# Kernel tuning notes

Measured on AMD Instinct MI355X. Metric: run time of the kernel, lower is better.

## Reference

```python
import jax, jax.numpy as jnp
import numpy as np

B, N, H, D = 8, 1024, 16, 64
HD = H * D

def setup_inputs() -> dict:
    key = jax.random.key(0)
    ks = jax.random.split(key, 7)
    return {
        "hidden_states": jax.random.normal(ks[0], (B, N, HD), dtype=jnp.float32),
        "qkv_w": jax.random.normal(ks[1], (3 * HD, HD), dtype=jnp.float32) * (HD ** -0.5),
        "q_bias": jax.random.normal(ks[2], (1, 1, HD), dtype=jnp.float32) * 0.02,
        "v_bias": jax.random.normal(ks[3], (1, 1, HD), dtype=jnp.float32) * 0.02,
        "rel_pos": jax.random.normal(ks[4], (1, H, N, N), dtype=jnp.float32),
        "rel_2d_pos": jax.random.normal(ks[5], (1, H, N, N), dtype=jnp.float32),
        "attention_mask": jax.random.randint(ks[6], (B, 1, 1, N), 0, 2, dtype=jnp.int32),
    }

def reference(hidden_states, qkv_w, q_bias, v_bias, rel_pos, rel_2d_pos, attention_mask):
    # fast_qkv path: fused projection, no bias in linear, then add q/v biases
    qkv = jnp.einsum("bnh,oh->bno", hidden_states, qkv_w)  # [B,N,3*HD]
    q, k, v = jnp.split(qkv, 3, axis=-1)
    q = q + q_bias
    v = v + v_bias

    def to_heads(x):  # [B,N,HD] -> [B,H,N,D]
        return x.reshape(B, N, H, D).transpose(0, 2, 1, 3)

    qh = to_heads(q) / jnp.sqrt(jnp.float32(D))
    kh = to_heads(k)
    vh = to_heads(v)

    scores = jnp.einsum("bhnd,bhmd->bhnm", qh, kh)  # [B,H,N,N]
    scores = scores + rel_pos + rel_2d_pos
    # torch mask_fill_ with value 1e-8 (NOT -inf) where mask is True
    scores = jnp.where(attention_mask.astype(bool), jnp.float32(1e-8), scores)
    probs = jax.nn.softmax(scores.astype(jnp.float32), axis=-1).astype(vh.dtype)
    # dropout prob = 0.0 (eval): identity
    ctx = jnp.einsum("bhnm,bhmd->bhnd", probs, vh)  # [B,H,N,D]
    ctx = ctx.transpose(0, 2, 1, 3).reshape(B, N, HD)
    return ctx
```

## Files before the change

### kernel.cpp

```cpp
#include <hip/hip_runtime.h>


typedef __bf16 bf16;
typedef __bf16 bf16x8 __attribute__((ext_vector_type(8)));
typedef __bf16 bf16x4 __attribute__((ext_vector_type(4)));
typedef float floatx4 __attribute__((ext_vector_type(4)));

#define MFMA16(a, b, c) __builtin_amdgcn_mfma_f32_16x16x32_bf16((a), (b), (c), 0, 0, 0)

#define LOG2E 1.4426950408889634f

#define GK(key) ((((key) ^ ((key) >> 3)) & 3) | (((((key) >> 2) ^ ((key) >> 3)) & 1) << 2))

__device__ __forceinline__ void gld16(const bf16* g, bf16* l) {
    __builtin_amdgcn_global_load_lds(
        (const __attribute__((address_space(1))) unsigned int*)g,
        (__attribute__((address_space(3))) unsigned int*)l, 16, 0, 0);
}

__global__ __launch_bounds__(256) void cvt_kernel(const float* __restrict__ x,
                                                  bf16* __restrict__ y, int n4) {
    int i = blockIdx.x * blockDim.x + threadIdx.x;
    if (i >= n4) return;
    float4 v = ((const float4*)x)[i];
    bf16x4 o;
    o.x = (bf16)v.x; o.y = (bf16)v.y; o.z = (bf16)v.z; o.w = (bf16)v.w;
    ((bf16x4*)y)[i] = o;
}

__global__ __launch_bounds__(256) void combine_kernel(const float* __restrict__ a,
                                                      const float* __restrict__ b,
                                                      bf16* __restrict__ y, int n4) {
    int i = blockIdx.x * blockDim.x + threadIdx.x;
    if (i >= n4) return;
    float4 va = ((const float4*)a)[i];
    float4 vb = ((const float4*)b)[i];
    bf16x4 o;
    o.x = (bf16)((va.x + vb.x) * LOG2E); o.y = (bf16)((va.y + vb.y) * LOG2E);
    o.z = (bf16)((va.z + vb.z) * LOG2E); o.w = (bf16)((va.w + vb.w) * LOG2E);
    ((bf16x4*)y)[i] = o;
}

__global__ __launch_bounds__(256) void mask64_kernel(const int* __restrict__ m,
                                                     unsigned long long* __restrict__ om64) {
    int tid = blockIdx.x * blockDim.x + threadIdx.x;
    int gw = tid >> 6, lane = tid & 63;
    bool keep = (m[gw * 64 + lane] == 0);
    unsigned long long bal = __ballot(keep);
    if (lane == 0) om64[gw] = bal;
}

__global__ __launch_bounds__(256) void qkv_gemm(
    const bf16* __restrict__ X, const bf16* __restrict__ W,
    const float* __restrict__ qbias, const float* __restrict__ vbias,
    bf16* __restrict__ qbuf, bf16* __restrict__ kbuf, bf16* __restrict__ vbuf) {
    __shared__ __align__(16) bf16 Al[128 * 32];
    __shared__ __align__(16) bf16 Bl[128 * 32];

    int tid = threadIdx.x, lane = tid & 63, w = tid >> 6;
    int quad = lane >> 4, lcol = lane & 15;
    int bx = blockIdx.x;
    int by = blockIdx.y;
    int wr = w >> 1, wc = w & 1;

    floatx4 z4 = {0.f, 0.f, 0.f, 0.f};
    floatx4 acc[4][4];
    for (int i = 0; i < 4; ++i)
        for (int j = 0; j < 4; ++j) acc[i][j] = z4;

    const bf16* Ag = X + (size_t)by * 128 * 1024;
    const bf16* Bg = W + (size_t)bx * 128 * 1024;

    for (int kt = 0; kt < 32; ++kt) {
        int k0 = kt * 32;
        __syncthreads();
        for (int j = 0; j < 2; ++j) {
            int c = (w * 2 + j) * 64 + lane;
            int row = c >> 2;
            int dc = (c & 3) ^ (row & 3);
            gld16(Ag + (size_t)row * 1024 + k0 + dc * 8, &Al[(w * 2 + j) * 64 * 8]);
        }
        for (int j = 0; j < 2; ++j) {
            int c = (w * 2 + j) * 64 + lane;
            int row = c >> 2;
            int dc = (c & 3) ^ (row & 3);
            gld16(Bg + (size_t)row * 1024 + k0 + dc * 8, &Bl[(w * 2 + j) * 64 * 8]);
        }
        __syncthreads();

        bf16x8 af[4], bfr[4];
        for (int i = 0; i < 4; ++i) {
            int r = wr * 64 + i * 16 + lcol;
            af[i] = *(const bf16x8*)&Al[r * 32 + ((quad ^ (r & 3)) * 8)];
        }
        for (int j = 0; j < 4; ++j) {
            int r = wc * 64 + j * 16 + lcol;
            bfr[j] = *(const bf16x8*)&Bl[r * 32 + ((quad ^ (r & 3)) * 8)];
        }
        for (int i = 0; i < 4; ++i)
            for (int j = 0; j < 4; ++j) acc[i][j] = MFMA16(af[i], bfr[j], acc[i][j]);
    }

    int col0 = bx * 128 + wc * 64;
    int row0 = by * 128 + wr * 64;
    int seg = col0 >> 10;

    for (int i = 0; i < 4; ++i) {
        int m0 = row0 + i * 16 + quad * 4;
        int bb = m0 >> 10, n0 = m0 & 1023;
        for (int j = 0; j < 4; ++j) {
            int o = col0 + j * 16 + lcol;
            if (seg == 0) {
                int hh = o >> 6, d = o & 63;
                float qb = qbias[o];
                for (int r = 0; r < 4; ++r) {
                    float v = (acc[i][j][r] + qb) * (0.125f * LOG2E);
                    qbuf[((size_t)((bb * 16 + hh) * 1024 + n0 + r)) * 64 + d] = (bf16)v;
                }
            } else if (seg == 1) {
                int o2 = o - 1024;
                int hh = o2 >> 6, d = o2 & 63;
                for (int r = 0; r < 4; ++r) {
                    kbuf[((size_t)((bb * 16 + hh) * 1024 + n0 + r)) * 64 + d] = (bf16)acc[i][j][r];
                }
            } else {
                int o2 = o - 2048;
                int hh = o2 >> 6, d = o2 & 63;
                float vbv = vbias[o2];
                bf16x4 pk;
                pk.x = (bf16)(acc[i][j][0] + vbv);
                pk.y = (bf16)(acc[i][j][1] + vbv);
                pk.z = (bf16)(acc[i][j][2] + vbv);
                pk.w = (bf16)(acc[i][j][3] + vbv);
                *(bf16x4*)&vbuf[((size_t)((bb * 16 + hh) * 64 + d)) * 1024 + n0] = pk;
            }
        }
    }
}

__global__ __launch_bounds__(256, 4) void flash_attn(
    const bf16* __restrict__ qbuf, const bf16* __restrict__ kbuf,
    const bf16* __restrict__ vbuf, const bf16* __restrict__ bias,
    const unsigned long long* __restrict__ om64, float* __restrict__ out) {
    __shared__ __align__(16) bf16 Kl[2][64 * 64];
    __shared__ __align__(16) bf16 Vl[2][64 * 64];

    int tid = threadIdx.x, lane = tid & 63, w = tid >> 6;
    int quad = lane >> 4, lcol = lane & 15;
    int bx = blockIdx.x;
    int xcd = bx & 7, slot = bx >> 3;
    int pair = xcd * 32 + (slot >> 3);
    int b = slot & 7;
    int h = pair >> 4, q4 = pair & 15;

    const bf16* kb = kbuf + ((size_t)((b * 16 + h) * 1024)) * 64;
    const bf16* vb = vbuf + ((size_t)((b * 16 + h) * 64)) * 1024;
    const unsigned long long* mp = om64 + b * 16;

    int qrow = q4 * 64 + w * 16;
    const bf16* qp = qbuf + ((size_t)((b * 16 + h) * 1024 + qrow + lcol)) * 64;
    bf16x8 qf0 = *(const bf16x8*)(qp + quad * 8);
    bf16x8 qf1 = *(const bf16x8*)(qp + 32 + quad * 8);
    const bf16* bb = bias + (size_t)h * 1024 * 1024 + (size_t)(qrow + lcol) * 1024;

    floatx4 z4 = {0.f, 0.f, 0.f, 0.f};
    floatx4 oacc[4] = {z4, z4, z4, z4};
    float lrun = 0.f;

#pragma unroll
    for (int j = 0; j < 2; ++j) {
        int c = (w * 2 + j) * 64 + lane;
        int key = c >> 3;
        int dc = (c & 7) ^ GK(key);
        gld16(kb + (size_t)key * 64 + dc * 8, &Kl[0][(w * 2 + j) * 512]);
    }
#pragma unroll
    for (int j = 0; j < 2; ++j) {
        int c = (w * 2 + j) * 64 + lane;
        int d = c >> 3;
        int kc = (c & 7) ^ (d & 7);
        gld16(vb + (size_t)d * 1024 + kc * 8, &Vl[0][(w * 2 + j) * 512]);
    }

    bf16x4 bf_[4];
#pragma unroll
    for (int j = 0; j < 4; ++j) {
        int kboff = ((j >> 1) << 5) + (quad << 3) + ((j & 1) << 2);
        bf_[j] = *(const bf16x4*)(bb + kboff);
    }
    unsigned long long mcur = mp[0];

    for (int kt = 0; kt < 16; ++kt) {
        int k0 = kt * 64;
        int cur = kt & 1, nxt = cur ^ 1;
        __syncthreads();

        if (kt < 15) {
            int k1 = k0 + 64;
#pragma unroll
            for (int j = 0; j < 2; ++j) {
                int c = (w * 2 + j) * 64 + lane;
                int key = c >> 3;
                int dc = (c & 7) ^ GK(key);
                gld16(kb + (size_t)(k1 + key) * 64 + dc * 8, &Kl[nxt][(w * 2 + j) * 512]);
            }
#pragma unroll
            for (int j = 0; j < 2; ++j) {
                int c = (w * 2 + j) * 64 + lane;
                int d = c >> 3;
                int kc = (c & 7) ^ (d & 7);
                gld16(vb + (size_t)d * 1024 + k1 + kc * 8, &Vl[nxt][(w * 2 + j) * 512]);
            }
        }
        int kp = (kt < 15) ? k0 + 64 : 0;
        bf16x4 bn[4];
#pragma unroll
        for (int j = 0; j < 4; ++j) {
            int kboff = ((j >> 1) << 5) + (quad << 3) + ((j & 1) << 2);
            bn[j] = *(const bf16x4*)(bb + kp + kboff);
        }
        unsigned long long mn = mp[(kt < 15) ? kt + 1 : 0];

        floatx4 sacc[4];
#pragma unroll
        for (int j = 0; j < 4; ++j) {
            int key = ((j >> 1) << 5) + ((lcol >> 2) << 3) + ((j & 1) << 2) + (lcol & 3);
            int gk = GK(key);
            bf16x8 kf0 = *(const bf16x8*)&Kl[cur][key * 64 + ((quad ^ gk) * 8)];
            bf16x8 kf1 = *(const bf16x8*)&Kl[cur][key * 64 + (((4 + quad) ^ gk) * 8)];
            floatx4 binit;
            binit[0] = (float)bf_[j][0]; binit[1] = (float)bf_[j][1];
            binit[2] = (float)bf_[j][2]; binit[3] = (float)bf_[j][3];
            sacc[j] = MFMA16(kf0, qf0, binit);
            sacc[j] = MFMA16(kf1, qf1, sacc[j]);
        }

        unsigned int mbits = ((unsigned int)(mcur >> (8 * quad)) & 0xffu) |
                             (((unsigned int)(mcur >> (32 + 8 * quad)) & 0xffu) << 8);
        float p[4][4];
        float psum = 0.f;
#pragma unroll
        for (int j = 0; j < 4; ++j)
#pragma unroll
            for (int r = 0; r < 4; ++r) {
                float sv = ((mbits >> (j * 4 + r)) & 1u) ? sacc[j][r] : 0.f;
                p[j][r] = __builtin_amdgcn_exp2f(sv);
                psum += p[j][r];
            }
        lrun += psum;

        bf16x8 pf0, pf1;
        pf0[0] = (bf16)p[0][0]; pf0[1] = (bf16)p[0][1];
        pf0[2] = (bf16)p[0][2]; pf0[3] = (bf16)p[0][3];
        pf0[4] = (bf16)p[1][0]; pf0[5] = (bf16)p[1][1];
        pf0[6] = (bf16)p[1][2]; pf0[7] = (bf16)p[1][3];
        pf1[0] = (bf16)p[2][0]; pf1[1] = (bf16)p[2][1];
        pf1[2] = (bf16)p[2][2]; pf1[3] = (bf16)p[2][3];
        pf1[4] = (bf16)p[3][0]; pf1[5] = (bf16)p[3][1];
        pf1[6] = (bf16)p[3][2]; pf1[7] = (bf16)p[3][3];

#pragma unroll
        for (int jd = 0; jd < 4; ++jd) {
            int dd = jd * 16 + lcol;
            bf16x8 vf0 = *(const bf16x8*)&Vl[cur][dd * 64 + ((quad ^ (dd & 7)) * 8)];
            bf16x8 vf1 = *(const bf16x8*)&Vl[cur][dd * 64 + (((4 + quad) ^ (dd & 7)) * 8)];
            oacc[jd] = MFMA16(vf0, pf0, oacc[jd]);
            oacc[jd] = MFMA16(vf1, pf1, oacc[jd]);
        }

#pragma unroll
        for (int j = 0; j < 4; ++j) bf_[j] = bn[j];
        mcur = mn;
    }

    float l = lrun;
    l += __shfl_xor(l, 16);
    l += __shfl_xor(l, 32);
    float linv = 1.f / l;
#pragma unroll
    for (int jd = 0; jd < 4; ++jd) {
        float4 st;
        st.x = oacc[jd][0] * linv;
        st.y = oacc[jd][1] * linv;
        st.z = oacc[jd][2] * linv;
        st.w = oacc[jd][3] * linv;
        *(float4*)&out[((size_t)(b * 1024 + qrow + lcol)) * 1024 + h * 64 + jd * 16 + quad * 4] = st;
    }
}

extern "C" void kernel_launch(void* const* d_in, const int* in_sizes, int n_in,
                              void* d_out, int out_size, void* d_ws, size_t ws_size,
                              hipStream_t stream) {
    const float* hs   = (const float*)d_in[0];
    const float* qkvw = (const float*)d_in[1];
    const float* qb   = (const float*)d_in[2];
    const float* vbi  = (const float*)d_in[3];
    const float* rel  = (const float*)d_in[4];
    const float* rel2 = (const float*)d_in[5];
    const int*   msk  = (const int*)d_in[6];
    float* out = (float*)d_out;

    char* w = (char*)d_ws;
    bf16* Xb = (bf16*)w;  w += (size_t)8388608 * 2;
    bf16* Wb = (bf16*)w;  w += (size_t)3145728 * 2;
    bf16* Bb = (bf16*)w;  w += (size_t)16777216 * 2;
    bf16* Qb = (bf16*)w;  w += (size_t)8388608 * 2;
    bf16* Kb = (bf16*)w;  w += (size_t)8388608 * 2;
    bf16* Vb = (bf16*)w;  w += (size_t)8388608 * 2;
    unsigned long long* OM = (unsigned long long*)w; w += (size_t)128 * 8;

    cvt_kernel<<<8388608 / 4 / 256, 256, 0, stream>>>(hs, Xb, 8388608 / 4);
    cvt_kernel<<<3145728 / 4 / 256, 256, 0, stream>>>(qkvw, Wb, 3145728 / 4);
    combine_kernel<<<16777216 / 4 / 256, 256, 0, stream>>>(rel, rel2, Bb, 16777216 / 4);
    mask64_kernel<<<32, 256, 0, stream>>>(msk, OM);
    qkv_gemm<<<dim3(24, 64), 256, 0, stream>>>(Xb, Wb, qb, vbi, Qb, Kb, Vb);
    flash_attn<<<2048, 256, 0, stream>>>(Qb, Kb, Vb, Bb, OM, out);
}
```

Baseline: 340.3 us.

## Double-buffer QKV GEMM LDS tiles and fuse prep kernels into one launch

Merges the two fp32-to-bf16 conversions, the rel_pos combine and the mask ballot into a single block-indexed prep kernel, which removes three kernel launches and their gaps. The QKV GEMM now uses two LDS buffers: the next K-tile is loaded while MFMAs run on the current one, with one barrier per iteration instead of two. The LDS swizzle gains an extra XOR term to reduce bank conflicts. LDS use doubles, and overlap may be lost if the compiler inserts a full vmcnt wait before the LDS reads.

```diff
diff --git a/kernel.cpp b/kernel.cpp
--- a/kernel.cpp
+++ b/kernel.cpp
@@ -18,44 +18,48 @@
         (__attribute__((address_space(3))) unsigned int*)l, 16, 0, 0);
 }
 
-__global__ __launch_bounds__(256) void cvt_kernel(const float* __restrict__ x,
-                                                  bf16* __restrict__ y, int n4) {
-    int i = blockIdx.x * blockDim.x + threadIdx.x;
-    if (i >= n4) return;
-    float4 v = ((const float4*)x)[i];
-    bf16x4 o;
-    o.x = (bf16)v.x; o.y = (bf16)v.y; o.z = (bf16)v.z; o.w = (bf16)v.w;
-    ((bf16x4*)y)[i] = o;
-}
-
-__global__ __launch_bounds__(256) void combine_kernel(const float* __restrict__ a,
-                                                      const float* __restrict__ b,
-                                                      bf16* __restrict__ y, int n4) {
-    int i = blockIdx.x * blockDim.x + threadIdx.x;
-    if (i >= n4) return;
-    float4 va = ((const float4*)a)[i];
-    float4 vb = ((const float4*)b)[i];
-    bf16x4 o;
-    o.x = (bf16)((va.x + vb.x) * LOG2E); o.y = (bf16)((va.y + vb.y) * LOG2E);
-    o.z = (bf16)((va.z + vb.z) * LOG2E); o.w = (bf16)((va.w + vb.w) * LOG2E);
-    ((bf16x4*)y)[i] = o;
-}
-
-__global__ __launch_bounds__(256) void mask64_kernel(const int* __restrict__ m,
-                                                     unsigned long long* __restrict__ om64) {
-    int tid = blockIdx.x * blockDim.x + threadIdx.x;
-    int gw = tid >> 6, lane = tid & 63;
-    bool keep = (m[gw * 64 + lane] == 0);
-    unsigned long long bal = __ballot(keep);
-    if (lane == 0) om64[gw] = bal;
+__global__ __launch_bounds__(256) void prep_kernel(
+    const float* __restrict__ hs, const float* __restrict__ qkvw,
+    const float* __restrict__ rel, const float* __restrict__ rel2,
+    const int* __restrict__ msk,
+    bf16* __restrict__ Xb, bf16* __restrict__ Wb, bf16* __restrict__ Bb,
+    unsigned long long* __restrict__ OM) {
+    int bid = blockIdx.x, t = threadIdx.x;
+    if (bid < 16384) {
+        int i = bid * 256 + t;
+        float4 va = ((const float4*)rel)[i];
+        float4 vb = ((const float4*)rel2)[i];
+        bf16x4 o;
+        o.x = (bf16)((va.x + vb.x) * LOG2E); o.y = (bf16)((va.y + vb.y) * LOG2E);
+        o.z = (bf16)((va.z + vb.z) * LOG2E); o.w = (bf16)((va.w + vb.w) * LOG2E);
+        ((bf16x4*)Bb)[i] = o;
+    } else if (bid < 24576) {
+        int i = (bid - 16384) * 256 + t;
+        float4 v = ((const float4*)hs)[i];
+        bf16x4 o;
+        o.x = (bf16)v.x; o.y = (bf16)v.y; o.z = (bf16)v.z; o.w = (bf16)v.w;
+        ((bf16x4*)Xb)[i] = o;
+    } else if (bid < 27648) {
+        int i = (bid - 24576) * 256 + t;
+        float4 v = ((const float4*)qkvw)[i];
+        bf16x4 o;
+        o.x = (bf16)v.x; o.y = (bf16)v.y; o.z = (bf16)v.z; o.w = (bf16)v.w;
+        ((bf16x4*)Wb)[i] = o;
+    } else {
+        int tid = (bid - 27648) * 256 + t;
+        int gw = tid >> 6, lane = tid & 63;
+        bool keep = (msk[gw * 64 + lane] == 0);
+        unsigned long long bal = __ballot(keep);
+        if (lane == 0) OM[gw] = bal;
+    }
 }
 
 __global__ __launch_bounds__(256) void qkv_gemm(
     const bf16* __restrict__ X, const bf16* __restrict__ W,
     const float* __restrict__ qbias, const float* __restrict__ vbias,
     bf16* __restrict__ qbuf, bf16* __restrict__ kbuf, bf16* __restrict__ vbuf) {
-    __shared__ __align__(16) bf16 Al[128 * 32];
-    __shared__ __align__(16) bf16 Bl[128 * 32];
+    __shared__ __align__(16) bf16 Al[2][128 * 32];
+    __shared__ __align__(16) bf16 Bl[2][128 * 32];
 
     int tid = threadIdx.x, lane = tid & 63, w = tid >> 6;
     int quad = lane >> 4, lcol = lane & 15;
@@ -71,33 +75,47 @@
     const bf16* Ag = X + (size_t)by * 128 * 1024;
     const bf16* Bg = W + (size_t)bx * 128 * 1024;
 
+#pragma unroll
+    for (int j = 0; j < 2; ++j) {
+        int c = (w * 2 + j) * 64 + lane;
+        int row = c >> 2;
+        int dc = (c & 3) ^ (row & 3) ^ ((row >> 2) & 3);
+        gld16(Ag + (size_t)row * 1024 + dc * 8, &Al[0][(w * 2 + j) * 512]);
+        gld16(Bg + (size_t)row * 1024 + dc * 8, &Bl[0][(w * 2 + j) * 512]);
+    }
+
     for (int kt = 0; kt < 32; ++kt) {
-        int k0 = kt * 32;
+        int cur = kt & 1, nxt = cur ^ 1;
         __syncthreads();
-        for (int j = 0; j < 2; ++j) {
-            int c = (w * 2 + j) * 64 + lane;
-            int row = c >> 2;
-            int dc = (c & 3) ^ (row & 3);
-            gld16(Ag + (size_t)row * 1024 + k0 + dc * 8, &Al[(w * 2 + j) * 64 * 8]);
-        }
-        for (int j = 0; j < 2; ++j) {
-            int c = (w * 2 + j) * 64 + lane;
-            int row = c >> 2;
-            int dc = (c & 3) ^ (row & 3);
-            gld16(Bg + (size_t)row * 1024 + k0 + dc * 8, &Bl[(w * 2 + j) * 64 * 8]);
-        }
-        __syncthreads();
+
+        if (kt < 31) {
+            int k1 = (kt + 1) * 32;
+#pragma unroll
+            for (int j = 0; j < 2; ++j) {
+                int c = (w * 2 + j) * 64 + lane;
+                int row = c >> 2;
+                int dc = (c & 3) ^ (row & 3) ^ ((row >> 2) & 3);
+                gld16(Ag + (size_t)row * 1024 + k1 + dc * 8, &Al[nxt][(w * 2 + j) * 512]);
+                gld16(Bg + (size_t)row * 1024 + k1 + dc * 8, &Bl[nxt][(w * 2 + j) * 512]);
+            }
+        }
 
         bf16x8 af[4], bfr[4];
+#pragma unroll
         for (int i = 0; i < 4; ++i) {
             int r = wr * 64 + i * 16 + lcol;
-            af[i] = *(const bf16x8*)&Al[r * 32 + ((quad ^ (r & 3)) * 8)];
-        }
+            int sl = quad ^ (r & 3) ^ ((r >> 2) & 3);
+            af[i] = *(const bf16x8*)&Al[cur][r * 32 + sl * 8];
+        }
+#pragma unroll
         for (int j = 0; j < 4; ++j) {
             int r = wc * 64 + j * 16 + lcol;
-            bfr[j] = *(const bf16x8*)&Bl[r * 32 + ((quad ^ (r & 3)) * 8)];
-        }
+            int sl = quad ^ (r & 3) ^ ((r >> 2) & 3);
+            bfr[j] = *(const bf16x8*)&Bl[cur][r * 32 + sl * 8];
+        }
+#pragma unroll
         for (int i = 0; i < 4; ++i)
+#pragma unroll
             for (int j = 0; j < 4; ++j) acc[i][j] = MFMA16(af[i], bfr[j], acc[i][j]);
     }
 
@@ -309,10 +327,7 @@
     bf16* Vb = (bf16*)w;  w += (size_t)8388608 * 2;
     unsigned long long* OM = (unsigned long long*)w; w += (size_t)128 * 8;
 
-    cvt_kernel<<<8388608 / 4 / 256, 256, 0, stream>>>(hs, Xb, 8388608 / 4);
-    cvt_kernel<<<3145728 / 4 / 256, 256, 0, stream>>>(qkvw, Wb, 3145728 / 4);
-    combine_kernel<<<16777216 / 4 / 256, 256, 0, stream>>>(rel, rel2, Bb, 16777216 / 4);
-    mask64_kernel<<<32, 256, 0, stream>>>(msk, OM);
+    prep_kernel<<<27680, 256, 0, stream>>>(hs, qkvw, rel, rel2, msk, Xb, Wb, Bb, OM);
     qkv_gemm<<<dim3(24, 64), 256, 0, stream>>>(Xb, Wb, qb, vbi, Qb, Kb, Vb);
     flash_attn<<<2048, 256, 0, stream>>>(Qb, Kb, Vb, Bb, OM, out);
 }
```

Measured after the change: 349.4 us. +2.7%, slower.

## Fuse relative-position bias combine into attention and merge prep kernels

Applied to the files above, without the earlier changes.

Drops the separate kernel that summed rel_pos and rel_2d_pos into a bf16 bias buffer. The attention kernel now reads both fp32 bias tensors directly, then adds, scales by log2e and converts them in registers. The two input conversions and the mask ballot are also merged into a single launch. This removes one full pass over the large bias tensors plus several launches. The cost is that attention reads twice as many bias bytes in fp32 per batch, and relies on L2 reuse across batch blocks on the same XCD to keep that traffic down.

```diff
diff --git a/kernel.cpp b/kernel.cpp
--- a/kernel.cpp
+++ b/kernel.cpp
@@ -18,36 +18,31 @@
         (__attribute__((address_space(3))) unsigned int*)l, 16, 0, 0);
 }
 
-__global__ __launch_bounds__(256) void cvt_kernel(const float* __restrict__ x,
-                                                  bf16* __restrict__ y, int n4) {
-    int i = blockIdx.x * blockDim.x + threadIdx.x;
-    if (i >= n4) return;
-    float4 v = ((const float4*)x)[i];
-    bf16x4 o;
-    o.x = (bf16)v.x; o.y = (bf16)v.y; o.z = (bf16)v.z; o.w = (bf16)v.w;
-    ((bf16x4*)y)[i] = o;
-}
-
-__global__ __launch_bounds__(256) void combine_kernel(const float* __restrict__ a,
-                                                      const float* __restrict__ b,
-                                                      bf16* __restrict__ y, int n4) {
-    int i = blockIdx.x * blockDim.x + threadIdx.x;
-    if (i >= n4) return;
-    float4 va = ((const float4*)a)[i];
-    float4 vb = ((const float4*)b)[i];
-    bf16x4 o;
-    o.x = (bf16)((va.x + vb.x) * LOG2E); o.y = (bf16)((va.y + vb.y) * LOG2E);
-    o.z = (bf16)((va.z + vb.z) * LOG2E); o.w = (bf16)((va.w + vb.w) * LOG2E);
-    ((bf16x4*)y)[i] = o;
-}
-
-__global__ __launch_bounds__(256) void mask64_kernel(const int* __restrict__ m,
-                                                     unsigned long long* __restrict__ om64) {
-    int tid = blockIdx.x * blockDim.x + threadIdx.x;
-    int gw = tid >> 6, lane = tid & 63;
-    bool keep = (m[gw * 64 + lane] == 0);
-    unsigned long long bal = __ballot(keep);
-    if (lane == 0) om64[gw] = bal;
+__global__ __launch_bounds__(256) void prep_kernel(
+    const float* __restrict__ hs, const float* __restrict__ qkvw,
+    const int* __restrict__ msk,
+    bf16* __restrict__ Xb, bf16* __restrict__ Wb,
+    unsigned long long* __restrict__ OM) {
+    int bid = blockIdx.x, t = threadIdx.x;
+    if (bid < 8192) {
+        int i = bid * 256 + t;
+        float4 v = ((const float4*)hs)[i];
+        bf16x4 o;
+        o.x = (bf16)v.x; o.y = (bf16)v.y; o.z = (bf16)v.z; o.w = (bf16)v.w;
+        ((bf16x4*)Xb)[i] = o;
+    } else if (bid < 11264) {
+        int i = (bid - 8192) * 256 + t;
+        float4 v = ((const float4*)qkvw)[i];
+        bf16x4 o;
+        o.x = (bf16)v.x; o.y = (bf16)v.y; o.z = (bf16)v.z; o.w = (bf16)v.w;
+        ((bf16x4*)Wb)[i] = o;
+    } else {
+        int tid = (bid - 11264) * 256 + t;
+        int gw = tid >> 6, lane = tid & 63;
+        bool keep = (msk[gw * 64 + lane] == 0);
+        unsigned long long bal = __ballot(keep);
+        if (lane == 0) OM[gw] = bal;
+    }
 }
 
 __global__ __launch_bounds__(256) void qkv_gemm(
@@ -140,7 +135,8 @@
 
 __global__ __launch_bounds__(256, 4) void flash_attn(
     const bf16* __restrict__ qbuf, const bf16* __restrict__ kbuf,
-    const bf16* __restrict__ vbuf, const bf16* __restrict__ bias,
+    const bf16* __restrict__ vbuf, const float* __restrict__ rel,
+    const float* __restrict__ rel2,
     const unsigned long long* __restrict__ om64, float* __restrict__ out) {
     __shared__ __align__(16) bf16 Kl[2][64 * 64];
     __shared__ __align__(16) bf16 Vl[2][64 * 64];
@@ -161,7 +157,8 @@
     const bf16* qp = qbuf + ((size_t)((b * 16 + h) * 1024 + qrow + lcol)) * 64;
     bf16x8 qf0 = *(const bf16x8*)(qp + quad * 8);
     bf16x8 qf1 = *(const bf16x8*)(qp + 32 + quad * 8);
-    const bf16* bb = bias + (size_t)h * 1024 * 1024 + (size_t)(qrow + lcol) * 1024;
+    const float* b0 = rel + (size_t)h * 1024 * 1024 + (size_t)(qrow + lcol) * 1024;
+    const float* b1 = rel2 + (size_t)h * 1024 * 1024 + (size_t)(qrow + lcol) * 1024;
 
     floatx4 z4 = {0.f, 0.f, 0.f, 0.f};
     floatx4 oacc[4] = {z4, z4, z4, z4};
@@ -186,7 +183,12 @@
 #pragma unroll
     for (int j = 0; j < 4; ++j) {
         int kboff = ((j >> 1) << 5) + (quad << 3) + ((j & 1) << 2);
-        bf_[j] = *(const bf16x4*)(bb + kboff);
+        floatx4 ra = *(const floatx4*)(b0 + kboff);
+        floatx4 rb = *(const floatx4*)(b1 + kboff);
+        bf_[j].x = (bf16)((ra[0] + rb[0]) * LOG2E);
+        bf_[j].y = (bf16)((ra[1] + rb[1]) * LOG2E);
+        bf_[j].z = (bf16)((ra[2] + rb[2]) * LOG2E);
+        bf_[j].w = (bf16)((ra[3] + rb[3]) * LOG2E);
     }
     unsigned long long mcur = mp[0];
 
@@ -217,7 +219,12 @@
 #pragma unroll
         for (int j = 0; j < 4; ++j) {
             int kboff = ((j >> 1) << 5) + (quad << 3) + ((j & 1) << 2);
-            bn[j] = *(const bf16x4*)(bb + kp + kboff);
+            floatx4 ra = *(const floatx4*)(b0 + kp + kboff);
+            floatx4 rb = *(const floatx4*)(b1 + kp + kboff);
+            bn[j].x = (bf16)((ra[0] + rb[0]) * LOG2E);
+            bn[j].y = (bf16)((ra[1] + rb[1]) * LOG2E);
+            bn[j].z = (bf16)((ra[2] + rb[2]) * LOG2E);
+            bn[j].w = (bf16)((ra[3] + rb[3]) * LOG2E);
         }
         unsigned long long mn = mp[(kt < 15) ? kt + 1 : 0];
 
@@ -303,16 +310,12 @@
     char* w = (char*)d_ws;
     bf16* Xb = (bf16*)w;  w += (size_t)8388608 * 2;
     bf16* Wb = (bf16*)w;  w += (size_t)3145728 * 2;
-    bf16* Bb = (bf16*)w;  w += (size_t)16777216 * 2;
     bf16* Qb = (bf16*)w;  w += (size_t)8388608 * 2;
     bf16* Kb = (bf16*)w;  w += (size_t)8388608 * 2;
     bf16* Vb = (bf16*)w;  w += (size_t)8388608 * 2;
     unsigned long long* OM = (unsigned long long*)w; w += (size_t)128 * 8;
 
-    cvt_kernel<<<8388608 / 4 / 256, 256, 0, stream>>>(hs, Xb, 8388608 / 4);
-    cvt_kernel<<<3145728 / 4 / 256, 256, 0, stream>>>(qkvw, Wb, 3145728 / 4);
-    combine_kernel<<<16777216 / 4 / 256, 256, 0, stream>>>(rel, rel2, Bb, 16777216 / 4);
-    mask64_kernel<<<32, 256, 0, stream>>>(msk, OM);
+    prep_kernel<<<11296, 256, 0, stream>>>(hs, qkvw, msk, Xb, Wb, OM);
     qkv_gemm<<<dim3(24, 64), 256, 0, stream>>>(Xb, Wb, qb, vbi, Qb, Kb, Vb);
-    flash_attn<<<2048, 256, 0, stream>>>(Qb, Kb, Vb, Bb, OM, out);
-}
+    flash_attn<<<2048, 256, 0, stream>>>(Qb, Kb, Vb, rel, rel2, OM, out);
+}
```

Measured after the change: 387.2 us. 1.14x slower.
